# Performance work log

Measured on AMD Instinct MI355X. Metric: run time of the kernel, lower is better.

Reference implementation:

```python
import jax, jax.numpy as jnp
import numpy as np

DS = 4  # pooling / upsample factor


def _avg_pool(t, ds):
    B, C, H, W = t.shape
    return t.reshape(B, C, H // ds, ds, W // ds, ds).mean(axis=(3, 5))


def setup_inputs() -> dict:
    key = jax.random.key(0)
    ks = jax.random.split(key, 8)
    B, C, H, W = 8, 512, 128, 128
    Ck = C // 4
    inp = jax.random.normal(ks[0], (B, C, H, W), dtype=jnp.float32)
    c2 = jax.random.normal(ks[1], (B, C, H, W), dtype=jnp.float32)
    # 1x1 conv weights == dense matrices over channel dim (with bias, as nn.Conv2d default)
    Wq = jax.random.normal(ks[2], (Ck, C), dtype=jnp.float32) * 0.02
    bq = jax.random.normal(ks[3], (Ck,), dtype=jnp.float32) * 0.02
    Wk = jax.random.normal(ks[4], (Ck, C), dtype=jnp.float32) * 0.02
    bk = jax.random.normal(ks[5], (Ck,), dtype=jnp.float32) * 0.02
    Wv = jax.random.normal(ks[6], (C, C), dtype=jnp.float32) * 0.02
    bv = jax.random.normal(ks[7], (C,), dtype=jnp.float32) * 0.02
    return {"input": inp, "c2": c2, "Wq": Wq, "bq": bq, "Wk": Wk, "bk": bk, "Wv": Wv, "bv": bv}


def reference(input, c2, Wq, bq, Wk, bk, Wv, bv):
    # Note: the torch module's `gamma` parameter is NOT used in forward; faithful omission.
    x = _avg_pool(input, DS)  # [B,C,h,w]
    y = _avg_pool(c2, DS)
    B, C, h, w = x.shape
    N = h * w
    Ck = Wq.shape[0]
    xf = x.reshape(B, C, N)
    yf = y.reshape(B, C, N)
    q = jnp.einsum('oc,bcn->bon', Wq, xf) + bq[None, :, None]  # [B,Ck,N]
    k = jnp.einsum('oc,bcn->bon', Wk, yf) + bk[None, :, None]  # [B,Ck,N]
    v = jnp.einsum('oc,bcn->bon', Wv, yf) + bv[None, :, None]  # [B,C,N]
    scale = jnp.asarray(Ck, x.dtype) ** -0.5
    energy = jnp.einsum('bon,bom->bnm', q, k) * scale  # [B,N,N] = q^T k
    attn = jax.nn.softmax(energy, axis=-1)
    out = jnp.einsum('bcm,bnm->bcn', v, attn)  # v @ attn^T
    out = out.reshape(B, C, h, w)
    # F.interpolate with default mode='nearest' and size = exact integer multiple -> repeat
    out = jnp.repeat(jnp.repeat(out, DS, axis=2), DS, axis=3)
    return out + c2
```

## Files before the change

kernel.cpp:

```cpp
#include <hip/hip_runtime.h>
#include <stdint.h>
#include <stddef.h>

#define Bn   8
#define Cn   512
#define CKn  128
#define Hn   128
#define Nn   1024

typedef float f32x4 __attribute__((ext_vector_type(4)));
typedef short bf16x8 __attribute__((ext_vector_type(8)));

__device__ __forceinline__ uint16_t f2b(float f) {
  uint32_t x = __float_as_uint(f);
  uint32_t r = (x + 0x7FFFu + ((x >> 16) & 1u)) >> 16;
  return (uint16_t)r;
}

__device__ __forceinline__ void gld_lds16(const uint16_t* g, short* lds_base, int lane) {
#if __has_builtin(__builtin_amdgcn_global_load_lds)
  __builtin_amdgcn_global_load_lds(
      (const __attribute__((address_space(1))) void*)g,
      (__attribute__((address_space(3))) void*)lds_base, 16, 0, 0);
#else
  *(bf16x8*)(lds_base + lane * 8) = *(const bf16x8*)g;
#endif
}

__device__ __forceinline__ void gemm64x128(const uint16_t* __restrict__ A,
                                           const uint16_t* __restrict__ Bt,
                                           int lda, int ldb, int K,
                                           short* As, short* Bs, f32x4 acc[8]) {
  const int tid  = threadIdx.x;
  const int lane = tid & 63;
  const int wave = tid >> 6;
  const int quad = lane >> 4, l16 = lane & 15;
  const int rin  = lane >> 2, cc = lane & 3;
  for (int kt = 0; kt < K; kt += 32) {
    __syncthreads();
    gld_lds16(A + (size_t)(wave * 16 + rin) * lda + kt + cc * 8, As + wave * 512, lane);
    gld_lds16(Bt + (size_t)(wave * 32 + rin) * ldb + kt + cc * 8, Bs + wave * 1024, lane);
    gld_lds16(Bt + (size_t)(wave * 32 + 16 + rin) * ldb + kt + cc * 8, Bs + wave * 1024 + 512, lane);
    __syncthreads();
    bf16x8 af = *(const bf16x8*)(As + (wave * 16 + l16) * 32 + quad * 8);
#pragma unroll
    for (int j = 0; j < 8; ++j) {
      bf16x8 bfr = *(const bf16x8*)(Bs + (j * 16 + l16) * 32 + quad * 8);
      acc[j] = __builtin_amdgcn_mfma_f32_16x16x32_bf16(af, bfr, acc[j], 0, 0, 0);
    }
  }
}

#define EPI_VARS \
  const int lane = threadIdx.x & 63; const int wave = threadIdx.x >> 6; \
  const int quad = lane >> 4, l16 = lane & 15;

__global__ __launch_bounds__(256) void wconv_kernel(
    const float* __restrict__ Wq, const float* __restrict__ Wk, const float* __restrict__ Wv,
    uint16_t* __restrict__ Wqb, uint16_t* __restrict__ Wkb, uint16_t* __restrict__ Wvb) {
  int i = blockIdx.x * 256 + threadIdx.x;
  if (i < CKn * Cn) { Wqb[i] = f2b(Wq[i]); Wkb[i] = f2b(Wk[i]); }
  Wvb[i] = f2b(Wv[i]);
}

__global__ __launch_bounds__(1024) void pool_kernel(
    const float* __restrict__ input, const float* __restrict__ c2,
    uint16_t* __restrict__ xT, uint16_t* __restrict__ yT) {
  const int cblk = blockIdx.x, ph = blockIdx.y;
  const int b = blockIdx.z >> 1, src = blockIdx.z & 1;
  const float* in = src ? c2 : input;
  uint16_t* out = src ? yT : xT;
  const int tw = threadIdx.x & 31, tc = threadIdx.x >> 5;
  const int c = cblk * 32 + tc;
  const float* p = in + (((size_t)(b * Cn + c) * Hn) + ph * 4) * Hn + tw * 4;
  float s = 0.f;
#pragma unroll
  for (int r = 0; r < 4; ++r) {
    float4 t = *(const float4*)(p + (size_t)r * Hn);
    s += t.x + t.y + t.z + t.w;
  }
  __shared__ float tile[32][33];
  tile[tw][tc] = s * 0.0625f;
  __syncthreads();
  const int tn = threadIdx.x >> 5, tcc = threadIdx.x & 31;
  out[((size_t)b * Nn + ph * 32 + tn) * Cn + cblk * 32 + tcc] = f2b(tile[tn][tcc]);
}

__global__ __launch_bounds__(256) void qkv_kernel(
    const uint16_t* __restrict__ Wqb, const uint16_t* __restrict__ Wkb, const uint16_t* __restrict__ Wvb,
    const float* __restrict__ bq, const float* __restrict__ bk, const float* __restrict__ bv,
    const uint16_t* __restrict__ xT, const uint16_t* __restrict__ yT,
    uint16_t* __restrict__ qT, uint16_t* __restrict__ kT, uint16_t* __restrict__ vm) {
  __shared__ short As[2048], Bs[4096];
  const int bx = blockIdx.x;
  const int b = bx / 96, r = bx % 96;
  const int mt = r >> 3, nt = r & 7;
  int op, mbase; const uint16_t* A; const float* bias;
  if (mt < 2)      { op = 0; mbase = mt * 64;       A = Wqb + (size_t)mbase * Cn; bias = bq; }
  else if (mt < 4) { op = 1; mbase = (mt - 2) * 64; A = Wkb + (size_t)mbase * Cn; bias = bk; }
  else             { op = 2; mbase = (mt - 4) * 64; A = Wvb + (size_t)mbase * Cn; bias = bv; }
  const uint16_t* Bt = ((op == 0) ? xT : yT) + (size_t)b * Nn * Cn + (size_t)nt * 128 * Cn;
  f32x4 acc[8];
#pragma unroll
  for (int j = 0; j < 8; ++j) acc[j] = (f32x4)0.f;
  gemm64x128(A, Bt, Cn, Cn, Cn, As, Bs, acc);
  EPI_VARS;
#pragma unroll
  for (int j = 0; j < 8; ++j)
#pragma unroll
    for (int rg = 0; rg < 4; ++rg) {
      int m = mbase + wave * 16 + quad * 4 + rg;
      int n = nt * 128 + j * 16 + l16;
      float val = acc[j][rg] + bias[m];
      if (op == 2) vm[(size_t)b * Cn * Nn + (size_t)m * Nn + n] = f2b(val);
      else {
        uint16_t* dst = (op == 0) ? qT : kT;
        dst[(size_t)b * Nn * CKn + (size_t)n * CKn + m] = f2b(val);
      }
    }
}

__global__ __launch_bounds__(256) void energy_kernel(
    const uint16_t* __restrict__ qT, const uint16_t* __restrict__ kT,
    float* __restrict__ energy) {
  __shared__ short As[2048], Bs[4096];
  const int bx = blockIdx.x;
  const int b = bx >> 7, r = bx & 127, mt = r >> 3, nt = r & 7;
  const uint16_t* A  = qT + (size_t)b * Nn * CKn + (size_t)mt * 64 * CKn;
  const uint16_t* Bt = kT + (size_t)b * Nn * CKn + (size_t)nt * 128 * CKn;
  f32x4 acc[8];
#pragma unroll
  for (int j = 0; j < 8; ++j) acc[j] = (f32x4)0.f;
  gemm64x128(A, Bt, CKn, CKn, CKn, As, Bs, acc);
  EPI_VARS;
  const float scale = 0.08838834764831845f;
#pragma unroll
  for (int j = 0; j < 8; ++j)
#pragma unroll
    for (int rg = 0; rg < 4; ++rg) {
      int n = mt * 64 + wave * 16 + quad * 4 + rg;
      int m = nt * 128 + j * 16 + l16;
      energy[(size_t)b * Nn * Nn + (size_t)n * Nn + m] = acc[j][rg] * scale;
    }
}

__global__ __launch_bounds__(256) void softmax_kernel(
    const float* __restrict__ energy, uint16_t* __restrict__ attn) {
  const size_t row = blockIdx.x;
  const float* e = energy + row * Nn;
  const int t = threadIdx.x;
  float v0[4];
  float mx = -3.4e38f;
#pragma unroll
  for (int i = 0; i < 4; ++i) { v0[i] = e[t + i * 256]; mx = fmaxf(mx, v0[i]); }
#pragma unroll
  for (int off = 32; off; off >>= 1) mx = fmaxf(mx, __shfl_xor(mx, off, 64));
  __shared__ float redm[4], reds[4];
  const int lane = t & 63, wave = t >> 6;
  if (lane == 0) redm[wave] = mx;
  __syncthreads();
  mx = fmaxf(fmaxf(redm[0], redm[1]), fmaxf(redm[2], redm[3]));
  float s = 0.f;
#pragma unroll
  for (int i = 0; i < 4; ++i) { v0[i] = __expf(v0[i] - mx); s += v0[i]; }
#pragma unroll
  for (int off = 32; off; off >>= 1) s += __shfl_xor(s, off, 64);
  if (lane == 0) reds[wave] = s;
  __syncthreads();
  s = reds[0] + reds[1] + reds[2] + reds[3];
  const float inv = 1.f / s;
#pragma unroll
  for (int i = 0; i < 4; ++i) attn[row * Nn + t + i * 256] = f2b(v0[i] * inv);
}

__global__ __launch_bounds__(256) void outg_kernel(
    const uint16_t* __restrict__ vm, const uint16_t* __restrict__ attn,
    float* __restrict__ osm) {
  __shared__ short As[2048], Bs[4096];
  const int bx = blockIdx.x;
  const int b = bx >> 6, r = bx & 63, mt = r >> 3, nt = r & 7;
  const uint16_t* A  = vm   + (size_t)b * Cn * Nn + (size_t)mt * 64 * Nn;
  const uint16_t* Bt = attn + (size_t)b * Nn * Nn + (size_t)nt * 128 * Nn;
  f32x4 acc[8];
#pragma unroll
  for (int j = 0; j < 8; ++j) acc[j] = (f32x4)0.f;
  gemm64x128(A, Bt, Nn, Nn, Nn, As, Bs, acc);
  EPI_VARS;
#pragma unroll
  for (int j = 0; j < 8; ++j)
#pragma unroll
    for (int rg = 0; rg < 4; ++rg) {
      int c = mt * 64 + wave * 16 + quad * 4 + rg;
      int n = nt * 128 + j * 16 + l16;
      osm[(size_t)b * Cn * Nn + (size_t)c * Nn + n] = acc[j][rg];
    }
}

__global__ __launch_bounds__(256) void upsample_kernel(
    const float* __restrict__ osm, const float* __restrict__ c2,
    float* __restrict__ out) {
  const int t = blockIdx.x * 256 + threadIdx.x;
  const int ww4 = t & 31;
  const int hh  = (t >> 5) & 127;
  const int cb  = t >> 12;
  const int n = (hh >> 2) * 32 + ww4;
  const float val = osm[((size_t)cb << 10) + n];
  const size_t base = (((size_t)cb * Hn) + hh) * Hn + ww4 * 4;
  float4 t4 = *(const float4*)(c2 + base);
  t4.x += val; t4.y += val; t4.z += val; t4.w += val;
  *(float4*)(out + base) = t4;
}

extern "C" void kernel_launch(void* const* d_in, const int* in_sizes, int n_in,
                              void* d_out, int out_size, void* d_ws, size_t ws_size,
                              hipStream_t stream) {
  const float* input = (const float*)d_in[0];
  const float* c2    = (const float*)d_in[1];
  const float* Wq    = (const float*)d_in[2];
  const float* bq    = (const float*)d_in[3];
  const float* Wk    = (const float*)d_in[4];
  const float* bk    = (const float*)d_in[5];
  const float* Wv    = (const float*)d_in[6];
  const float* bv    = (const float*)d_in[7];
  float* out = (float*)d_out;
  uint8_t* ws = (uint8_t*)d_ws;

  uint16_t* xT   = (uint16_t*)(ws + 0);
  uint16_t* yT   = (uint16_t*)(ws + 8388608);
  uint16_t* Wqb  = (uint16_t*)(ws + 16777216);
  uint16_t* Wkb  = (uint16_t*)(ws + 16908288);
  uint16_t* Wvb  = (uint16_t*)(ws + 17039360);
  uint16_t* qT   = (uint16_t*)(ws + 17563648);
  uint16_t* kT   = (uint16_t*)(ws + 19660800);
  uint16_t* vm   = (uint16_t*)(ws + 21757952);
  float*    eng  = (float*)   (ws + 30146560);
  uint16_t* attn = (uint16_t*)(ws + 63700992);
  float*    osm  = eng;

  hipLaunchKernelGGL(wconv_kernel, dim3(1024), dim3(256), 0, stream,
                     Wq, Wk, Wv, Wqb, Wkb, Wvb);
  hipLaunchKernelGGL(pool_kernel, dim3(16, 32, 16), dim3(1024), 0, stream,
                     input, c2, xT, yT);
  hipLaunchKernelGGL(qkv_kernel, dim3(768), dim3(256), 0, stream,
                     Wqb, Wkb, Wvb, bq, bk, bv, xT, yT, qT, kT, vm);
  hipLaunchKernelGGL(energy_kernel, dim3(1024), dim3(256), 0, stream, qT, kT, eng);
  hipLaunchKernelGGL(softmax_kernel, dim3(8192), dim3(256), 0, stream, eng, attn);
  hipLaunchKernelGGL(outg_kernel, dim3(512), dim3(256), 0, stream, vm, attn, osm);
  hipLaunchKernelGGL(upsample_kernel, dim3(65536), dim3(256), 0, stream, osm, c2, out);
}
```

Baseline: 704.6 us.

## Fuse energy+softmax and output GEMM+upsample, enlarge GEMM tiles to 128x128

Energy GEMM and softmax are merged into one kernel that computes a 16-row strip across all 1024 keys and normalizes in registers, so the fp32 energy matrix is never written to or read from global memory. The output GEMM now adds c2 and performs the nearest upsample in its epilogue, removing the osm buffer and a separate launch. The shared GEMM helper moves from a 64x128 to a 128x128 block tile with a 2x2 wave layout, improving operand reuse. In exchange, outup launches only 256 blocks, which may underfill the GPU, and its epilogue writes are strided per element.

```diff
diff --git a/kernel.cpp b/kernel.cpp
--- a/kernel.cpp
+++ b/kernel.cpp
@@ -27,33 +27,42 @@
 #endif
 }
 
-__device__ __forceinline__ void gemm64x128(const uint16_t* __restrict__ A,
-                                           const uint16_t* __restrict__ Bt,
-                                           int lda, int ldb, int K,
-                                           short* As, short* Bs, f32x4 acc[8]) {
+__device__ __forceinline__ void gemm128(const uint16_t* __restrict__ A,
+                                        const uint16_t* __restrict__ Bt,
+                                        int lda, int ldb, int K,
+                                        short* As, short* Bs, f32x4 acc[4][4]) {
   const int tid  = threadIdx.x;
   const int lane = tid & 63;
   const int wave = tid >> 6;
   const int quad = lane >> 4, l16 = lane & 15;
   const int rin  = lane >> 2, cc = lane & 3;
+  const int wr = wave >> 1, wc = wave & 1;
   for (int kt = 0; kt < K; kt += 32) {
     __syncthreads();
-    gld_lds16(A + (size_t)(wave * 16 + rin) * lda + kt + cc * 8, As + wave * 512, lane);
-    gld_lds16(Bt + (size_t)(wave * 32 + rin) * ldb + kt + cc * 8, Bs + wave * 1024, lane);
+    gld_lds16(A  + (size_t)(wave * 32 +      rin) * lda + kt + cc * 8, As + wave * 1024,       lane);
+    gld_lds16(A  + (size_t)(wave * 32 + 16 + rin) * lda + kt + cc * 8, As + wave * 1024 + 512, lane);
+    gld_lds16(Bt + (size_t)(wave * 32 +      rin) * ldb + kt + cc * 8, Bs + wave * 1024,       lane);
     gld_lds16(Bt + (size_t)(wave * 32 + 16 + rin) * ldb + kt + cc * 8, Bs + wave * 1024 + 512, lane);
     __syncthreads();
-    bf16x8 af = *(const bf16x8*)(As + (wave * 16 + l16) * 32 + quad * 8);
-#pragma unroll
-    for (int j = 0; j < 8; ++j) {
-      bf16x8 bfr = *(const bf16x8*)(Bs + (j * 16 + l16) * 32 + quad * 8);
-      acc[j] = __builtin_amdgcn_mfma_f32_16x16x32_bf16(af, bfr, acc[j], 0, 0, 0);
-    }
+    bf16x8 af[4], bfr[4];
+#pragma unroll
+    for (int i = 0; i < 4; ++i)
+      af[i] = *(const bf16x8*)(As + (wr * 64 + i * 16 + l16) * 32 + quad * 8);
+#pragma unroll
+    for (int j = 0; j < 4; ++j)
+      bfr[j] = *(const bf16x8*)(Bs + (wc * 64 + j * 16 + l16) * 32 + quad * 8);
+#pragma unroll
+    for (int i = 0; i < 4; ++i)
+#pragma unroll
+      for (int j = 0; j < 4; ++j)
+        acc[i][j] = __builtin_amdgcn_mfma_f32_16x16x32_bf16(af[i], bfr[j], acc[i][j], 0, 0, 0);
   }
 }
 
 #define EPI_VARS \
   const int lane = threadIdx.x & 63; const int wave = threadIdx.x >> 6; \
-  const int quad = lane >> 4, l16 = lane & 15;
+  const int quad = lane >> 4, l16 = lane & 15; \
+  const int wr = wave >> 1, wc = wave & 1;
 
 __global__ __launch_bounds__(256) void wconv_kernel(
     const float* __restrict__ Wq, const float* __restrict__ Wk, const float* __restrict__ Wv,
@@ -91,124 +100,157 @@
     const float* __restrict__ bq, const float* __restrict__ bk, const float* __restrict__ bv,
     const uint16_t* __restrict__ xT, const uint16_t* __restrict__ yT,
     uint16_t* __restrict__ qT, uint16_t* __restrict__ kT, uint16_t* __restrict__ vm) {
-  __shared__ short As[2048], Bs[4096];
-  const int bx = blockIdx.x;
-  const int b = bx / 96, r = bx % 96;
+  __shared__ short As[4096], Bs[4096];
+  const int b = blockIdx.y;
+  const int r = blockIdx.x;
   const int mt = r >> 3, nt = r & 7;
-  int op, mbase; const uint16_t* A; const float* bias;
-  if (mt < 2)      { op = 0; mbase = mt * 64;       A = Wqb + (size_t)mbase * Cn; bias = bq; }
-  else if (mt < 4) { op = 1; mbase = (mt - 2) * 64; A = Wkb + (size_t)mbase * Cn; bias = bk; }
-  else             { op = 2; mbase = (mt - 4) * 64; A = Wvb + (size_t)mbase * Cn; bias = bv; }
+  int op, m0; const uint16_t* A; const float* bias;
+  if (mt == 0)      { op = 0; m0 = 0;              A = Wqb;                     bias = bq; }
+  else if (mt == 1) { op = 1; m0 = 0;              A = Wkb;                     bias = bk; }
+  else              { op = 2; m0 = (mt - 2) * 128; A = Wvb + (size_t)m0 * Cn;   bias = bv; }
   const uint16_t* Bt = ((op == 0) ? xT : yT) + (size_t)b * Nn * Cn + (size_t)nt * 128 * Cn;
-  f32x4 acc[8];
-#pragma unroll
-  for (int j = 0; j < 8; ++j) acc[j] = (f32x4)0.f;
-  gemm64x128(A, Bt, Cn, Cn, Cn, As, Bs, acc);
+  f32x4 acc[4][4];
+#pragma unroll
+  for (int i = 0; i < 4; ++i)
+#pragma unroll
+    for (int j = 0; j < 4; ++j) acc[i][j] = (f32x4)0.f;
+  gemm128(A, Bt, Cn, Cn, Cn, As, Bs, acc);
   EPI_VARS;
 #pragma unroll
-  for (int j = 0; j < 8; ++j)
+  for (int i = 0; i < 4; ++i)
+#pragma unroll
+    for (int j = 0; j < 4; ++j)
+#pragma unroll
+      for (int rg = 0; rg < 4; ++rg) {
+        int m = m0 + wr * 64 + i * 16 + quad * 4 + rg;
+        int n = nt * 128 + wc * 64 + j * 16 + l16;
+        float val = acc[i][j][rg] + bias[m];
+        if (op == 2) vm[(size_t)(b * Cn + m) * Nn + n] = f2b(val);
+        else {
+          uint16_t* dst = (op == 0) ? qT : kT;
+          dst[(size_t)(b * Nn + n) * CKn + m] = f2b(val);
+        }
+      }
+}
+
+__global__ __launch_bounds__(1024) void esm_kernel(
+    const uint16_t* __restrict__ qT, const uint16_t* __restrict__ kT,
+    uint16_t* __restrict__ attn) {
+  const int b = blockIdx.y, n0 = blockIdx.x * 16;
+  const int tid = threadIdx.x, lane = tid & 63, w = tid >> 6;
+  const int quad = lane >> 4, l16 = lane & 15;
+  const uint16_t* qb = qT + (size_t)(b * Nn + n0) * CKn;
+  const uint16_t* kb = kT + (size_t)(b * Nn + w * 64) * CKn;
+  f32x4 acc[4];
+#pragma unroll
+  for (int j = 0; j < 4; ++j) acc[j] = (f32x4)0.f;
+#pragma unroll
+  for (int kt = 0; kt < CKn; kt += 32) {
+    bf16x8 af = *(const bf16x8*)(qb + (size_t)l16 * CKn + kt + quad * 8);
+    bf16x8 bfr[4];
+#pragma unroll
+    for (int j = 0; j < 4; ++j)
+      bfr[j] = *(const bf16x8*)(kb + (size_t)(j * 16 + l16) * CKn + kt + quad * 8);
+#pragma unroll
+    for (int j = 0; j < 4; ++j)
+      acc[j] = __builtin_amdgcn_mfma_f32_16x16x32_bf16(af, bfr[j], acc[j], 0, 0, 0);
+  }
+  const float scale = 0.08838834764831845f;
+#pragma unroll
+  for (int j = 0; j < 4; ++j) acc[j] *= scale;
+
+  __shared__ float red[16][16];
+  __shared__ float gout[16];
+  float mx[4];
+#pragma unroll
+  for (int rg = 0; rg < 4; ++rg) {
+    mx[rg] = fmaxf(fmaxf(acc[0][rg], acc[1][rg]), fmaxf(acc[2][rg], acc[3][rg]));
+#pragma unroll
+    for (int off = 1; off < 16; off <<= 1) mx[rg] = fmaxf(mx[rg], __shfl_xor(mx[rg], off, 64));
+  }
+  if (l16 == 0) {
+#pragma unroll
+    for (int rg = 0; rg < 4; ++rg) red[quad * 4 + rg][w] = mx[rg];
+  }
+  __syncthreads();
+  if (tid < 16) {
+    float g = -3.4e38f;
+#pragma unroll
+    for (int ww = 0; ww < 16; ++ww) g = fmaxf(g, red[tid][ww]);
+    gout[tid] = g;
+  }
+  __syncthreads();
+  float rmax[4];
+#pragma unroll
+  for (int rg = 0; rg < 4; ++rg) rmax[rg] = gout[quad * 4 + rg];
+  float sm[4] = {0.f, 0.f, 0.f, 0.f};
+#pragma unroll
+  for (int j = 0; j < 4; ++j)
 #pragma unroll
     for (int rg = 0; rg < 4; ++rg) {
-      int m = mbase + wave * 16 + quad * 4 + rg;
-      int n = nt * 128 + j * 16 + l16;
-      float val = acc[j][rg] + bias[m];
-      if (op == 2) vm[(size_t)b * Cn * Nn + (size_t)m * Nn + n] = f2b(val);
-      else {
-        uint16_t* dst = (op == 0) ? qT : kT;
-        dst[(size_t)b * Nn * CKn + (size_t)n * CKn + m] = f2b(val);
+      float p = __expf(acc[j][rg] - rmax[rg]);
+      acc[j][rg] = p;
+      sm[rg] += p;
+    }
+#pragma unroll
+  for (int rg = 0; rg < 4; ++rg)
+#pragma unroll
+    for (int off = 1; off < 16; off <<= 1) sm[rg] += __shfl_xor(sm[rg], off, 64);
+  if (l16 == 0) {
+#pragma unroll
+    for (int rg = 0; rg < 4; ++rg) red[quad * 4 + rg][w] = sm[rg];
+  }
+  __syncthreads();
+  if (tid < 16) {
+    float s = 0.f;
+#pragma unroll
+    for (int ww = 0; ww < 16; ++ww) s += red[tid][ww];
+    gout[tid] = 1.f / s;
+  }
+  __syncthreads();
+#pragma unroll
+  for (int rg = 0; rg < 4; ++rg) {
+    float inv = gout[quad * 4 + rg];
+    uint16_t* arow = attn + (size_t)(b * Nn + n0 + quad * 4 + rg) * Nn + w * 64;
+#pragma unroll
+    for (int j = 0; j < 4; ++j) arow[j * 16 + l16] = f2b(acc[j][rg] * inv);
+  }
+}
+
+__global__ __launch_bounds__(256) void outup_kernel(
+    const uint16_t* __restrict__ vm, const uint16_t* __restrict__ attn,
+    const float* __restrict__ c2, float* __restrict__ out) {
+  __shared__ short As[4096], Bs[4096];
+  const int b = blockIdx.y;
+  const int r = blockIdx.x, mt = r >> 3, nt = r & 7;
+  const uint16_t* A  = vm   + (size_t)b * Cn * Nn + (size_t)mt * 128 * Nn;
+  const uint16_t* Bt = attn + (size_t)b * Nn * Nn + (size_t)nt * 128 * Nn;
+  f32x4 acc[4][4];
+#pragma unroll
+  for (int i = 0; i < 4; ++i)
+#pragma unroll
+    for (int j = 0; j < 4; ++j) acc[i][j] = (f32x4)0.f;
+  gemm128(A, Bt, Nn, Nn, Nn, As, Bs, acc);
+  EPI_VARS;
+#pragma unroll
+  for (int i = 0; i < 4; ++i)
+#pragma unroll
+    for (int j = 0; j < 4; ++j) {
+      const int n  = nt * 128 + wc * 64 + j * 16 + l16;
+      const int ph = n >> 5, pw = n & 31;
+#pragma unroll
+      for (int rg = 0; rg < 4; ++rg) {
+        const int c = mt * 128 + wr * 64 + i * 16 + quad * 4 + rg;
+        const float v = acc[i][j][rg];
+        const size_t base = (((size_t)(b * Cn + c) * Hn) + ph * 4) * Hn + pw * 4;
+#pragma unroll
+        for (int rr = 0; rr < 4; ++rr) {
+          float4 t4 = *(const float4*)(c2 + base + (size_t)rr * Hn);
+          t4.x += v; t4.y += v; t4.z += v; t4.w += v;
+          *(float4*)(out + base + (size_t)rr * Hn) = t4;
+        }
       }
     }
-}
-
-__global__ __launch_bounds__(256) void energy_kernel(
-    const uint16_t* __restrict__ qT, const uint16_t* __restrict__ kT,
-    float* __restrict__ energy) {
-  __shared__ short As[2048], Bs[4096];
-  const int bx = blockIdx.x;
-  const int b = bx >> 7, r = bx & 127, mt = r >> 3, nt = r & 7;
-  const uint16_t* A  = qT + (size_t)b * Nn * CKn + (size_t)mt * 64 * CKn;
-  const uint16_t* Bt = kT + (size_t)b * Nn * CKn + (size_t)nt * 128 * CKn;
-  f32x4 acc[8];
-#pragma unroll
-  for (int j = 0; j < 8; ++j) acc[j] = (f32x4)0.f;
-  gemm64x128(A, Bt, CKn, CKn, CKn, As, Bs, acc);
-  EPI_VARS;
-  const float scale = 0.08838834764831845f;
-#pragma unroll
-  for (int j = 0; j < 8; ++j)
-#pragma unroll
-    for (int rg = 0; rg < 4; ++rg) {
-      int n = mt * 64 + wave * 16 + quad * 4 + rg;
-      int m = nt * 128 + j * 16 + l16;
-      energy[(size_t)b * Nn * Nn + (size_t)n * Nn + m] = acc[j][rg] * scale;
-    }
-}
-
-__global__ __launch_bounds__(256) void softmax_kernel(
-    const float* __restrict__ energy, uint16_t* __restrict__ attn) {
-  const size_t row = blockIdx.x;
-  const float* e = energy + row * Nn;
-  const int t = threadIdx.x;
-  float v0[4];
-  float mx = -3.4e38f;
-#pragma unroll
-  for (int i = 0; i < 4; ++i) { v0[i] = e[t + i * 256]; mx = fmaxf(mx, v0[i]); }
-#pragma unroll
-  for (int off = 32; off; off >>= 1) mx = fmaxf(mx, __shfl_xor(mx, off, 64));
-  __shared__ float redm[4], reds[4];
-  const int lane = t & 63, wave = t >> 6;
-  if (lane == 0) redm[wave] = mx;
-  __syncthreads();
-  mx = fmaxf(fmaxf(redm[0], redm[1]), fmaxf(redm[2], redm[3]));
-  float s = 0.f;
-#pragma unroll
-  for (int i = 0; i < 4; ++i) { v0[i] = __expf(v0[i] - mx); s += v0[i]; }
-#pragma unroll
-  for (int off = 32; off; off >>= 1) s += __shfl_xor(s, off, 64);
-  if (lane == 0) reds[wave] = s;
-  __syncthreads();
-  s = reds[0] + reds[1] + reds[2] + reds[3];
-  const float inv = 1.f / s;
-#pragma unroll
-  for (int i = 0; i < 4; ++i) attn[row * Nn + t + i * 256] = f2b(v0[i] * inv);
-}
-
-__global__ __launch_bounds__(256) void outg_kernel(
-    const uint16_t* __restrict__ vm, const uint16_t* __restrict__ attn,
-    float* __restrict__ osm) {
-  __shared__ short As[2048], Bs[4096];
-  const int bx = blockIdx.x;
-  const int b = bx >> 6, r = bx & 63, mt = r >> 3, nt = r & 7;
-  const uint16_t* A  = vm   + (size_t)b * Cn * Nn + (size_t)mt * 64 * Nn;
-  const uint16_t* Bt = attn + (size_t)b * Nn * Nn + (size_t)nt * 128 * Nn;
-  f32x4 acc[8];
-#pragma unroll
-  for (int j = 0; j < 8; ++j) acc[j] = (f32x4)0.f;
-  gemm64x128(A, Bt, Nn, Nn, Nn, As, Bs, acc);
-  EPI_VARS;
-#pragma unroll
-  for (int j = 0; j < 8; ++j)
-#pragma unroll
-    for (int rg = 0; rg < 4; ++rg) {
-      int c = mt * 64 + wave * 16 + quad * 4 + rg;
-      int n = nt * 128 + j * 16 + l16;
-      osm[(size_t)b * Cn * Nn + (size_t)c * Nn + n] = acc[j][rg];
-    }
-}
-
-__global__ __launch_bounds__(256) void upsample_kernel(
-    const float* __restrict__ osm, const float* __restrict__ c2,
-    float* __restrict__ out) {
-  const int t = blockIdx.x * 256 + threadIdx.x;
-  const int ww4 = t & 31;
-  const int hh  = (t >> 5) & 127;
-  const int cb  = t >> 12;
-  const int n = (hh >> 2) * 32 + ww4;
-  const float val = osm[((size_t)cb << 10) + n];
-  const size_t base = (((size_t)cb * Hn) + hh) * Hn + ww4 * 4;
-  float4 t4 = *(const float4*)(c2 + base);
-  t4.x += val; t4.y += val; t4.z += val; t4.w += val;
-  *(float4*)(out + base) = t4;
 }
 
 extern "C" void kernel_launch(void* const* d_in, const int* in_sizes, int n_in,
@@ -233,18 +275,15 @@
   uint16_t* qT   = (uint16_t*)(ws + 17563648);
   uint16_t* kT   = (uint16_t*)(ws + 19660800);
   uint16_t* vm   = (uint16_t*)(ws + 21757952);
-  float*    eng  = (float*)   (ws + 30146560);
-  uint16_t* attn = (uint16_t*)(ws + 63700992);
-  float*    osm  = eng;
+  uint16_t* attn = (uint16_t*)(ws + 30146560);
 
   hipLaunchKernelGGL(wconv_kernel, dim3(1024), dim3(256), 0, stream,
                      Wq, Wk, Wv, Wqb, Wkb, Wvb);
   hipLaunchKernelGGL(pool_kernel, dim3(16, 32, 16), dim3(1024), 0, stream,
                      input, c2, xT, yT);
-  hipLaunchKernelGGL(qkv_kernel, dim3(768), dim3(256), 0, stream,
+  hipLaunchKernelGGL(qkv_kernel, dim3(48, 8), dim3(256), 0, stream,
                      Wqb, Wkb, Wvb, bq, bk, bv, xT, yT, qT, kT, vm);
-  hipLaunchKernelGGL(energy_kernel, dim3(1024), dim3(256), 0, stream, qT, kT, eng);
-  hipLaunchKernelGGL(softmax_kernel, dim3(8192), dim3(256), 0, stream, eng, attn);
-  hipLaunchKernelGGL(outg_kernel, dim3(512), dim3(256), 0, stream, vm, attn, osm);
-  hipLaunchKernelGGL(upsample_kernel, dim3(65536), dim3(256), 0, stream, osm, c2, out);
-}
+  hipLaunchKernelGGL(esm_kernel, dim3(64, 8), dim3(1024), 0, stream, qT, kT, attn);
+  hipLaunchKernelGGL(outup_kernel, dim3(32, 8), dim3(256), 0, stream,
+                     vm, attn, c2, out);
+}
```

Result: slower. 722.9 us (+2.6%).
